# Performance work log

Measured on AMD Instinct MI355X. Metric: run time of the kernel, lower is better.

The kernel has to match this reference:

```python
import jax, jax.numpy as jnp
import numpy as np
from jax import lax

DIM = 192; HEADS = 6; WS = 7; SS = 3; D = H = W = 28
N = WS ** 3            # 343 tokens per window
L = D * H * W          # 21952 tokens
B = 2; HID = 4 * DIM   # 768
SCALE = (DIM // HEADS) ** -0.5
EPS = 1e-5


def _win_part_np(x, ws):
    Bn, Hh, Ww, Tt, C = x.shape
    x = x.reshape(Bn, Hh // ws, ws, Ww // ws, ws, Tt // ws, ws, C)
    return x.transpose(0, 1, 3, 5, 2, 4, 6, 7).reshape(-1, ws, ws, ws, C)


def build_mask():
    # standard Swin shifted-window mask: region ids -> pairwise -100/0
    img = np.zeros((1, D, H, W, 1), np.float32)
    cnt = 0
    sls = (slice(0, -WS), slice(-WS, -SS), slice(-SS, None))
    for a in sls:
        for b in sls:
            for c in sls:
                img[:, a, b, c, :] = cnt
                cnt += 1
    mw = _win_part_np(img, WS).reshape(-1, N)  # (nW, N)
    am = mw[:, None, :] - mw[:, :, None]
    return np.where(am != 0, -100.0, 0.0).astype(np.float32)


def _rel_pos_index():
    coords = np.stack(np.meshgrid(np.arange(WS), np.arange(WS), np.arange(WS), indexing='ij'))
    cf = coords.reshape(3, -1)
    rc = (cf[:, :, None] - cf[:, None, :]).transpose(1, 2, 0)
    rc += WS - 1
    rc[..., 0] *= (2 * WS - 1) ** 2
    rc[..., 1] *= (2 * WS - 1)
    return rc.sum(-1)  # (N, N)

RPI = jnp.asarray(_rel_pos_index())


def setup_inputs() -> dict:
    key = jax.random.key(0)
    ks = jax.random.split(key, 12)
    p = lambda i, shape: jax.random.normal(ks[i], shape, jnp.float32) * 0.02
    return dict(
        x=jax.random.normal(ks[0], (B, L, DIM), jnp.float32),
        mask_matrixx=jnp.asarray(build_mask()),
        norm1_g=jnp.ones((DIM,), jnp.float32), norm1_b=jnp.zeros((DIM,), jnp.float32),
        qkv_w=p(1, (DIM, 3 * DIM)), qkv_b=jnp.zeros((3 * DIM,), jnp.float32),
        rpb=p(2, ((2 * WS - 1) ** 3, HEADS)),
        proj_w=p(3, (DIM, DIM)), proj_b=jnp.zeros((DIM,), jnp.float32),
        norm2_g=jnp.ones((DIM,), jnp.float32), norm2_b=jnp.zeros((DIM,), jnp.float32),
        lin1_w=p(4, (DIM, HID)), lin1_b=jnp.zeros((HID,), jnp.float32),
        lin2_w=p(5, (HID, DIM)), lin2_b=jnp.zeros((DIM,), jnp.float32),
        dw1_k=p(6, (DIM, 1, 3, 3, 3)), dw1_b=jnp.zeros((DIM,), jnp.float32),
        pw1_k=p(7, (DIM, DIM, 1, 1, 1)), pw1_b=jnp.zeros((DIM,), jnp.float32),
        dw2_k=p(8, (DIM, 1, 3, 3, 3)), dw2_b=jnp.zeros((DIM,), jnp.float32),
        pw2_k=p(9, (DIM, DIM, 1, 1, 1)), pw2_b=jnp.zeros((DIM,), jnp.float32),
    )


def _ln(x, g, b):
    m = x.mean(-1, keepdims=True)
    v = ((x - m) ** 2).mean(-1, keepdims=True)
    return (x - m) * lax.rsqrt(v + EPS) * g + b


def _conv3d(x, k, b, groups):
    y = lax.conv_general_dilated(x, k, (1, 1, 1), 'SAME', feature_group_count=groups,
                                 dimension_numbers=('NCDHW', 'OIDHW', 'NCDHW'))
    return y + b.reshape(1, -1, 1, 1, 1)


def reference(x, mask_matrixx, norm1_g, norm1_b, qkv_w, qkv_b, rpb, proj_w, proj_b,
              norm2_g, norm2_b, lin1_w, lin1_b, lin2_w, lin2_b,
              dw1_k, dw1_b, pw1_k, pw1_b, dw2_k, dw2_b, pw2_k, pw2_b):
    shortcut = x
    xn = _ln(x, norm1_g, norm1_b).reshape(B, D, H, W, DIM)
    # cyclic shift (shift_size > 0)
    sx = jnp.roll(xn, (-SS, -SS, -SS), axis=(1, 2, 3))
    # window partition -> (B*nW, N, C)
    xw = sx.reshape(B, D // WS, WS, H // WS, WS, W // WS, WS, DIM)
    xw = xw.transpose(0, 1, 3, 5, 2, 4, 6, 7).reshape(-1, N, DIM)
    Bw = xw.shape[0]
    nW = Bw // B
    hd = DIM // HEADS
    qkv = (xw @ qkv_w + qkv_b).reshape(Bw, N, 3, HEADS, hd).transpose(2, 0, 3, 1, 4)
    q, k, v = qkv[0] * SCALE, qkv[1], qkv[2]
    attn = jnp.einsum('bhnd,bhmd->bhnm', q, k)
    attn = attn + rpb[RPI].transpose(2, 0, 1)[None]          # (1, heads, N, N)
    attn = attn.reshape(B, nW, HEADS, N, N) + mask_matrixx[None, :, None]
    attn = jax.nn.softmax(attn.reshape(Bw, HEADS, N, N), axis=-1)
    out = jnp.einsum('bhnm,bhmd->bhnd', attn, v).transpose(0, 2, 1, 3).reshape(Bw, N, DIM)
    out = out @ proj_w + proj_b
    # window reverse + reverse shift
    out = out.reshape(B, D // WS, H // WS, W // WS, WS, WS, WS, DIM)
    out = out.transpose(0, 1, 4, 2, 5, 3, 6, 7).reshape(B, D, H, W, DIM)
    out = jnp.roll(out, (SS, SS, SS), axis=(1, 2, 3)).reshape(B, L, DIM)
    x = shortcut + out
    # LeFeedForward: linear MLP branch + double depthwise-separable conv3d branch
    xm = _ln(x, norm2_g, norm2_b)
    lin = jax.nn.gelu(xm @ lin1_w + lin1_b, approximate=False) @ lin2_w + lin2_b
    rx = xm.reshape(B, D, H, W, DIM).transpose(0, 4, 1, 2, 3)  # NCDHW
    rx = _conv3d(_conv3d(rx, dw1_k, dw1_b, DIM), pw1_k, pw1_b, 1)
    rx = _conv3d(_conv3d(rx, dw2_k, dw2_b, DIM), pw2_k, pw2_b, 1)
    # original does rx.view(B, -1, dim) on NCDHW-contiguous memory (layout-mixing);
    # jnp.reshape on the same layout replicates it exactly
    rx = rx.reshape(B, -1, DIM)
    return x + (rx + lin)
```

## Files before the change

### kernel.cpp

```cpp
#include <hip/hip_runtime.h>

typedef unsigned short u16;
typedef unsigned int   u32;

#define DIMC 192
#define NWIN 343
#define LTOK 21952
#define ROWSZ 43904
#define TOTE 8429568
#define QSCALE 0.17677669529663689f
#define EPSF 1e-5f

typedef __attribute__((ext_vector_type(8))) short bf16x8v;
typedef __attribute__((ext_vector_type(4))) float f32x4v;

__device__ __forceinline__ float bu(u16 v){ union{u32 u; float f;} x; x.u = ((u32)v)<<16; return x.f; }
__device__ __forceinline__ float lo16(u32 p){ union{u32 u; float f;} x; x.u = p<<16; return x.f; }
__device__ __forceinline__ float hi16(u32 p){ union{u32 u; float f;} x; x.u = p & 0xffff0000u; return x.f; }
__device__ __forceinline__ u16 fb(float f){
  union{float ff; u32 u;} x; x.ff = f;
  u32 r = (x.u + 0x7fffu + ((x.u>>16)&1u)) >> 16;
  return (u16)r;
}
__device__ __forceinline__ float gelu_f(float x){ return 0.5f*x*(1.0f + erff(x*0.70710678118654752f)); }

__device__ __forceinline__ f32x4v mfma_bf16(bf16x8v a, bf16x8v b, f32x4v c){
  return __builtin_amdgcn_mfma_f32_16x16x32_bf16(a, b, c, 0, 0, 0);
}

__device__ __forceinline__ void row_to_token(int row, int& b, int& l){
  int bw = row / NWIN, n = row % NWIN;
  b = bw >> 6; int wi = bw & 63;
  int sd = (wi>>4)*7      + n/49;
  int sh = ((wi>>2)&3)*7  + (n/7)%7;
  int sw = (wi&3)*7       + n%7;
  int d = sd+3; if(d>=28) d-=28;
  int h = sh+3; if(h>=28) h-=28;
  int w = sw+3; if(w>=28) w-=28;
  l = d*784 + h*28 + w;
}

template<int TR>
__global__ __launch_bounds__(256) void pack_w(const float* __restrict__ W, u16* __restrict__ dst,
                                              int K, int N){
  int gid = blockIdx.x*256 + threadIdx.x;
  if(gid >= K*N) return;
  int k = gid / N, n = gid - k*N;
  float v = TR ? W[(long)n*K + k] : W[(long)k*N + n];
  int nt = n >> 4, ks = k >> 5;
  int l  = (((k>>3)&3)<<4) | (n&15);
  int j  = k & 7;
  int KS = K >> 5;
  dst[((((nt*KS + ks)<<6) + l)<<3) + j] = fb(v);
}

__global__ __launch_bounds__(256) void pack_dwk(const float* __restrict__ k1, const float* __restrict__ k2,
                                                float* __restrict__ d1, float* __restrict__ d2){
  int gid = blockIdx.x*256 + threadIdx.x;
  if(gid < 5184){
    int tap = gid/192, c = gid - tap*192;
    d1[gid] = k1[c*27 + tap];
    d2[gid] = k2[c*27 + tap];
  }
}

__global__ __launch_bounds__(256) void ln_win(const float* __restrict__ x, const float* __restrict__ g,
                                              const float* __restrict__ bb, u16* __restrict__ out){
  int row  = blockIdx.x*4 + (threadIdx.x>>6);
  int lane = threadIdx.x & 63;
  int b, l; row_to_token(row, b, l);
  const float* p = x + ((long)b*LTOK + l)*DIMC;
  float v0 = p[lane], v1 = p[lane+64], v2 = p[lane+128];
  float s = v0+v1+v2;
  #pragma unroll
  for(int m=1;m<64;m<<=1) s += __shfl_xor(s,m);
  float mean = s*(1.f/192.f);
  float d0=v0-mean, d1=v1-mean, d2=v2-mean;
  float q = d0*d0+d1*d1+d2*d2;
  #pragma unroll
  for(int m=1;m<64;m<<=1) q += __shfl_xor(q,m);
  float rstd = rsqrtf(q*(1.f/192.f)+EPSF);
  u16* o = out + (long)row*DIMC;
  o[lane]     = fb(d0*rstd*g[lane]     + bb[lane]);
  o[lane+64]  = fb(d1*rstd*g[lane+64]  + bb[lane+64]);
  o[lane+128] = fb(d2*rstd*g[lane+128] + bb[lane+128]);
}

__global__ __launch_bounds__(256) void ln_plain(const u16* __restrict__ in, const float* __restrict__ g,
                                                const float* __restrict__ bb, u16* __restrict__ out){
  int row  = blockIdx.x*4 + (threadIdx.x>>6);
  int lane = threadIdx.x & 63;
  const u16* p = in + (long)row*DIMC;
  float v0 = bu(p[lane]), v1 = bu(p[lane+64]), v2 = bu(p[lane+128]);
  float s = v0+v1+v2;
  #pragma unroll
  for(int m=1;m<64;m<<=1) s += __shfl_xor(s,m);
  float mean = s*(1.f/192.f);
  float d0=v0-mean, d1=v1-mean, d2=v2-mean;
  float q = d0*d0+d1*d1+d2*d2;
  #pragma unroll
  for(int m=1;m<64;m<<=1) q += __shfl_xor(q,m);
  float rstd = rsqrtf(q*(1.f/192.f)+EPSF);
  u16* o = out + (long)row*DIMC;
  o[lane]     = fb(d0*rstd*g[lane]     + bb[lane]);
  o[lane+64]  = fb(d1*rstd*g[lane+64]  + bb[lane+64]);
  o[lane+128] = fb(d2*rstd*g[lane+128] + bb[lane+128]);
}

template<int NTOT, int EPI>
__global__ __launch_bounds__(256) void gemm_mfma(const u16* __restrict__ A, const u16* __restrict__ Wp,
                                                 const float* __restrict__ bias, u16* __restrict__ out,
                                                 const float* __restrict__ resid){
  constexpr int KS  = 6;
  constexpr int NPW = NTOT/64;
  __shared__ u16 As[32*192];
  const int tid = threadIdx.x;
  const int w = tid>>6, l = tid&63;
  const int lm = l&15, lh = l>>4;
  const long row0 = (long)blockIdx.x*32;

  {
    const uint4* src = (const uint4*)(A + row0*192);
    #pragma unroll
    for(int c=0;c<3;c++){
      int cz = tid + c*256;
      int row = cz/24;
      int byte = (cz*16) ^ ((row&7)<<4);
      *(uint4*)((char*)As + byte) = src[cz];
    }
  }
  __syncthreads();

  f32x4v acc[NPW][2];
  const f32x4v z4 = {0.f,0.f,0.f,0.f};
  #pragma unroll
  for(int i=0;i<NPW;i++){ acc[i][0]=z4; acc[i][1]=z4; }

  #pragma unroll
  for(int ks=0;ks<KS;ks++){
    bf16x8v a[2];
    #pragma unroll
    for(int mt=0;mt<2;mt++){
      int row = mt*16 + lm;
      int byte = (row*384 + ks*64 + lh*16) ^ ((row&7)<<4);
      a[mt] = *(const bf16x8v*)((const char*)As + byte);
    }
    #pragma unroll
    for(int i=0;i<NPW;i++){
      int nt = w*NPW + i;
      bf16x8v b = *(const bf16x8v*)(Wp + ((((nt*KS + ks)<<6) + l)<<3));
      acc[i][0] = mfma_bf16(a[0], b, acc[i][0]);
      acc[i][1] = mfma_bf16(a[1], b, acc[i][1]);
    }
  }

  #pragma unroll
  for(int i=0;i<NPW;i++){
    int n = (w*NPW + i)*16 + lm;
    float bv = bias[n];
    #pragma unroll
    for(int mt=0;mt<2;mt++){
      #pragma unroll
      for(int r=0;r<4;r++){
        long mrow = row0 + mt*16 + lh*4 + r;
        float v = acc[i][mt][r] + bv;
        if constexpr(EPI==0){
          out[mrow*NTOT + n] = fb(v);
        } else {
          int b_, lt; row_to_token((int)mrow, b_, lt);
          long li = ((long)b_*LTOK + lt)*DIMC + n;
          out[li] = fb(v + resid[li]);
        }
      }
    }
  }
}

__global__ __launch_bounds__(256) void mlp_mfma(const u16* __restrict__ xm, const u16* __restrict__ Wp1,
                                                const float* __restrict__ b1, const u16* __restrict__ Wp2,
                                                const float* __restrict__ b2, u16* __restrict__ out){
  __shared__ u16 As[32*192];
  __shared__ u16 Hs[32*768];
  const int tid = threadIdx.x;
  const int w = tid>>6, l = tid&63;
  const int lm = l&15, lh = l>>4;
  const long row0 = (long)blockIdx.x*32;

  {
    const uint4* src = (const uint4*)(xm + row0*192);
    #pragma unroll
    for(int c=0;c<3;c++){
      int cz = tid + c*256;
      int row = cz/24;
      int byte = (cz*16) ^ ((row&7)<<4);
      *(uint4*)((char*)As + byte) = src[cz];
    }
  }
  __syncthreads();

  const f32x4v z4 = {0.f,0.f,0.f,0.f};
  f32x4v acc1[12][2];
  #pragma unroll
  for(int i=0;i<12;i++){ acc1[i][0]=z4; acc1[i][1]=z4; }

  #pragma unroll
  for(int ks=0;ks<6;ks++){
    bf16x8v a[2];
    #pragma unroll
    for(int mt=0;mt<2;mt++){
      int row = mt*16 + lm;
      int byte = (row*384 + ks*64 + lh*16) ^ ((row&7)<<4);
      a[mt] = *(const bf16x8v*)((const char*)As + byte);
    }
    #pragma unroll
    for(int i=0;i<12;i++){
      int nt = w*12 + i;
      bf16x8v b = *(const bf16x8v*)(Wp1 + ((((nt*6 + ks)<<6) + l)<<3));
      acc1[i][0] = mfma_bf16(a[0], b, acc1[i][0]);
      acc1[i][1] = mfma_bf16(a[1], b, acc1[i][1]);
    }
  }

  #pragma unroll
  for(int i=0;i<12;i++){
    int n = (w*12 + i)*16 + lm;
    float bv = b1[n];
    #pragma unroll
    for(int mt=0;mt<2;mt++){
      #pragma unroll
      for(int r=0;r<4;r++){
        int mrow = mt*16 + lh*4 + r;
        float h = gelu_f(acc1[i][mt][r] + bv);
        int byte = (mrow*1536 + n*2) ^ ((mrow&7)<<4);
        *(u16*)((char*)Hs + byte) = fb(h);
      }
    }
  }
  __syncthreads();

  f32x4v acc2[3][2];
  #pragma unroll
  for(int i=0;i<3;i++){ acc2[i][0]=z4; acc2[i][1]=z4; }

  #pragma unroll 4
  for(int ks=0;ks<24;ks++){
    bf16x8v a[2];
    #pragma unroll
    for(int mt=0;mt<2;mt++){
      int row = mt*16 + lm;
      int byte = (row*1536 + ks*64 + lh*16) ^ ((row&7)<<4);
      a[mt] = *(const bf16x8v*)((const char*)Hs + byte);
    }
    #pragma unroll
    for(int i=0;i<3;i++){
      int nt = w*3 + i;
      bf16x8v b = *(const bf16x8v*)(Wp2 + ((((nt*24 + ks)<<6) + l)<<3));
      acc2[i][0] = mfma_bf16(a[0], b, acc2[i][0]);
      acc2[i][1] = mfma_bf16(a[1], b, acc2[i][1]);
    }
  }

  #pragma unroll
  for(int i=0;i<3;i++){
    int n = (w*3 + i)*16 + lm;
    float bv = b2[n];
    #pragma unroll
    for(int mt=0;mt<2;mt++){
      #pragma unroll
      for(int r=0;r<4;r++){
        long mrow = row0 + mt*16 + lh*4 + r;
        out[mrow*192 + n] = fb(acc2[i][mt][r] + bv);
      }
    }
  }
}

__global__ __launch_bounds__(256) void attn_mfma(const u16* __restrict__ qkv, const float* __restrict__ rpb,
                                                 u16* __restrict__ out){
  __shared__ u16 Qs[352*32];
  __shared__ u16 Ks2[352*32];
  __shared__ u16 Vt[32*360];
  __shared__ u16 Ps[4][16*360];
  __shared__ float rpb_l[2197];
  __shared__ u16 reg_l[352];

  const int tid = threadIdx.x;
  const int bw = blockIdx.x / 6, hh = blockIdx.x % 6;
  const int wi = bw & 63;
  const long rowbase = (long)bw*NWIN;

  for(int i=tid;i<2197;i+=256) rpb_l[i] = rpb[i*6+hh];
  for(int i2=tid;i2<352;i2+=256){
    int rg = 0;
    if(i2 < 343){
      int sd = (wi>>4)*7      + i2/49;
      int sh = ((wi>>2)&3)*7  + (i2/7)%7;
      int sw = (wi&3)*7       + i2%7;
      int rd = sd<21?0:(sd<25?1:2);
      int rh = sh<21?0:(sh<25?1:2);
      int rw = sw<21?0:(sw<25?1:2);
      rg = rd*9+rh*3+rw;
    }
    reg_l[i2] = (u16)rg;
  }
  if(tid < 144){ ((u32*)Qs)[343*16 + tid] = 0; ((u32*)Ks2)[343*16 + tid] = 0; }
  for(int p2=tid;p2<288;p2+=256){
    int d = p2/9, j = 343 + p2%9; Vt[d*360 + j] = 0;
  }

  for(int p = tid; p < 343*16; p += 256){
    int j = p >> 4, dp = p & 15;
    const u32* src = (const u32*)(qkv + (rowbase + j)*576 + hh*32) + dp;
    ((u32*)Qs)[j*16 + dp]  = src[0];
    ((u32*)Ks2)[j*16 + dp] = src[96];
    u32 vv = src[192];
    Vt[(dp*2)*360 + j]   = (u16)(vv & 0xffffu);
    Vt[(dp*2+1)*360 + j] = (u16)(vv >> 16);
  }
  __syncthreads();

  const int w = tid>>6, l = tid&63;
  const int lm = l&15, lh = l>>4;
  u16* Pw = Ps[w];
  const f32x4v z4 = {0.f,0.f,0.f,0.f};

  for(int it = w; it < 22; it += 4){
    const int i0 = it*16;
    bf16x8v aq = *(const bf16x8v*)(Qs + (i0+lm)*32 + lh*8);
    f32x4v acc[22];
    #pragma unroll
    for(int jt=0;jt<22;jt++){
      bf16x8v bk = *(const bf16x8v*)(Ks2 + (jt*16+lm)*32 + lh*8);
      acc[jt] = mfma_bf16(aq, bk, z4);
    }

    int izr[4], iyr[4], ixr[4], irr[4];
    #pragma unroll
    for(int r=0;r<4;r++){
      int i = i0 + lh*4 + r; if(i>342) i=342;
      izr[r]=i/49; int rem=i-izr[r]*49; iyr[r]=rem/7; ixr[r]=rem-iyr[r]*7;
      irr[r]=reg_l[i];
    }
    #pragma unroll
    for(int jt=0;jt<22;jt++){
      int j = jt*16 + lm;
      int jc = j>342?342:j;
      int jz=jc/49; int rem=jc-jz*49; int jy=rem/7; int jx=rem-jy*7;
      int rj = reg_l[jc];
      bool jok = j<343;
      #pragma unroll
      for(int r=0;r<4;r++){
        float bias = rpb_l[(izr[r]-jz+6)*169 + (iyr[r]-jy+6)*13 + (ixr[r]-jx+6)];
        float v = acc[jt][r]*QSCALE + bias + ((irr[r]==rj)?0.f:-100.f);
        acc[jt][r] = jok ? v : -1e30f;
      }
    }

    float rinv[4];
    #pragma unroll
    for(int r=0;r<4;r++){
      float mx = acc[0][r];
      #pragma unroll
      for(int jt=1;jt<22;jt++) mx = fmaxf(mx, acc[jt][r]);
      #pragma unroll
      for(int m=1;m<16;m<<=1) mx = fmaxf(mx, __shfl_xor(mx, m));
      float sm = 0.f;
      #pragma unroll
      for(int jt=0;jt<22;jt++){ float e = __expf(acc[jt][r]-mx); acc[jt][r]=e; sm += e; }
      #pragma unroll
      for(int m=1;m<16;m<<=1) sm += __shfl_xor(sm, m);
      rinv[r] = 1.0f/sm;
    }

    #pragma unroll
    for(int jt=0;jt<22;jt++){
      int j = jt*16+lm;
      #pragma unroll
      for(int r=0;r<4;r++) Pw[(lh*4+r)*360 + j] = fb(acc[jt][r]);
    }

    f32x4v o0=z4, o1=z4;
    #pragma unroll
    for(int ks=0;ks<11;ks++){
      bf16x8v ap = *(const bf16x8v*)(Pw + lm*360 + ks*32 + lh*8);
      bf16x8v b0 = *(const bf16x8v*)(Vt + lm*360 + ks*32 + lh*8);
      bf16x8v b1 = *(const bf16x8v*)(Vt + (16+lm)*360 + ks*32 + lh*8);
      o0 = mfma_bf16(ap, b0, o0);
      o1 = mfma_bf16(ap, b1, o1);
    }

    #pragma unroll
    for(int r=0;r<4;r++){
      int i = i0 + lh*4 + r;
      if(i < 343){
        u16* po = out + (rowbase + i)*192 + hh*32;
        po[lm]    = fb(o0[r]*rinv[r]);
        po[16+lm] = fb(o1[r]*rinv[r]);
      }
    }
  }
}

__global__ __launch_bounds__(256) void dw3v(const u16* __restrict__ in, const float* __restrict__ kwT,
                                            const float* __restrict__ bias, u16* __restrict__ out){
  __shared__ float wls[5184];
  const int tid = threadIdx.x;
  for(int i=tid;i<5184;i+=256) wls[i] = kwT[i];
  __syncthreads();

  int gid = blockIdx.x*256 + tid;
  int t  = gid / 24, c8 = gid - t*24;
  int b  = t / LTOK, s = t - b*LTOK;
  int z  = s / 784; int r2 = s - z*784; int y = r2/28; int x = r2 - y*28;
  const u16* base = in + (long)t*192 + c8*8;

  float acc[8];
  {
    const float4* bp = (const float4*)(bias + c8*8);
    float4 b0 = bp[0], b1 = bp[1];
    acc[0]=b0.x; acc[1]=b0.y; acc[2]=b0.z; acc[3]=b0.w;
    acc[4]=b1.x; acc[5]=b1.y; acc[6]=b1.z; acc[7]=b1.w;
  }

  #pragma unroll
  for(int dz=-1;dz<=1;dz++){
    int zz=z+dz; if((unsigned)zz>=28u) continue;
    #pragma unroll
    for(int dy=-1;dy<=1;dy++){
      int yy=y+dy; if((unsigned)yy>=28u) continue;
      #pragma unroll
      for(int dx=-1;dx<=1;dx++){
        int xx=x+dx; if((unsigned)xx>=28u) continue;
        int tap = (dz+1)*9+(dy+1)*3+(dx+1);
        uint4 v = *(const uint4*)(base + (long)(dz*784+dy*28+dx)*192);
        const float* wp = &wls[tap*192 + c8*8];
        float4 w0 = *(const float4*)wp;
        float4 w1 = *(const float4*)(wp+4);
        acc[0] = fmaf(lo16(v.x), w0.x, acc[0]);
        acc[1] = fmaf(hi16(v.x), w0.y, acc[1]);
        acc[2] = fmaf(lo16(v.y), w0.z, acc[2]);
        acc[3] = fmaf(hi16(v.y), w0.w, acc[3]);
        acc[4] = fmaf(lo16(v.z), w1.x, acc[4]);
        acc[5] = fmaf(hi16(v.z), w1.y, acc[5]);
        acc[6] = fmaf(lo16(v.w), w1.z, acc[6]);
        acc[7] = fmaf(hi16(v.w), w1.w, acc[7]);
      }
    }
  }

  uint4 o;
  o.x = ((u32)fb(acc[1])<<16) | fb(acc[0]);
  o.y = ((u32)fb(acc[3])<<16) | fb(acc[2]);
  o.z = ((u32)fb(acc[5])<<16) | fb(acc[4]);
  o.w = ((u32)fb(acc[7])<<16) | fb(acc[6]);
  *(uint4*)(out + (long)t*192 + c8*8) = o;
}

__global__ __launch_bounds__(256) void final_add(const u16* __restrict__ x1, const u16* __restrict__ lin,
                                                 const u16* __restrict__ t2, float* __restrict__ out){
  int gid = blockIdx.x*256 + threadIdx.x;
  int b  = gid / 4214784;
  int gg = gid - b*4214784;
  int ch = gg / LTOK;
  int sp = gg - ch*LTOK;
  out[gid] = bu(x1[gid]) + bu(lin[gid]) + bu(t2[((long)b*LTOK + sp)*192 + ch]);
}

extern "C" void kernel_launch(void* const* d_in, const int* in_sizes, int n_in,
                              void* d_out, int out_size, void* d_ws, size_t ws_size,
                              hipStream_t stream){
  const float* x      = (const float*)d_in[0];
  const float* n1g    = (const float*)d_in[2];
  const float* n1b    = (const float*)d_in[3];
  const float* qkv_w  = (const float*)d_in[4];
  const float* qkv_b  = (const float*)d_in[5];
  const float* rpb    = (const float*)d_in[6];
  const float* proj_w = (const float*)d_in[7];
  const float* proj_b = (const float*)d_in[8];
  const float* n2g    = (const float*)d_in[9];
  const float* n2b    = (const float*)d_in[10];
  const float* l1w    = (const float*)d_in[11];
  const float* l1b    = (const float*)d_in[12];
  const float* l2w    = (const float*)d_in[13];
  const float* l2b    = (const float*)d_in[14];
  const float* dw1k   = (const float*)d_in[15];
  const float* dw1b   = (const float*)d_in[16];
  const float* pw1k   = (const float*)d_in[17];
  const float* pw1b   = (const float*)d_in[18];
  const float* dw2k   = (const float*)d_in[19];
  const float* dw2b   = (const float*)d_in[20];
  const float* pw2k   = (const float*)d_in[21];
  const float* pw2b   = (const float*)d_in[22];

  const size_t FB = (size_t)ROWSZ * DIMC;
  u16* x1b   = (u16*)d_ws;
  u16* winb  = x1b + FB;
  u16* attnb = winb + FB;
  u16* qkvb  = attnb + FB;
  u16* cb1   = qkvb;
  u16* cb2   = qkvb + FB;
  u16* xmb   = winb;
  u16* linb  = attnb;
  u16* pk_qkv  = x1b + 6*FB;
  u16* pk_proj = pk_qkv  + 110592;
  u16* pk_l1   = pk_proj + 36864;
  u16* pk_l2   = pk_l1   + 147456;
  u16* pk_pw1  = pk_l2   + 147456;
  u16* pk_pw2  = pk_pw1  + 36864;
  float* kwT1  = (float*)(pk_pw2 + 36864);
  float* kwT2  = kwT1 + 5184;

  pack_w<0><<<432,256,0,stream>>>(qkv_w,  pk_qkv,  192, 576);
  pack_w<0><<<144,256,0,stream>>>(proj_w, pk_proj, 192, 192);
  pack_w<0><<<576,256,0,stream>>>(l1w,    pk_l1,   192, 768);
  pack_w<0><<<576,256,0,stream>>>(l2w,    pk_l2,   768, 192);
  pack_w<1><<<144,256,0,stream>>>(pw1k,   pk_pw1,  192, 192);
  pack_w<1><<<144,256,0,stream>>>(pw2k,   pk_pw2,  192, 192);
  pack_dwk<<<21,256,0,stream>>>(dw1k, dw2k, kwT1, kwT2);

  ln_win<<<ROWSZ/4,256,0,stream>>>(x, n1g, n1b, winb);
  gemm_mfma<576,0><<<ROWSZ/32,256,0,stream>>>(winb, pk_qkv, qkv_b, qkvb, nullptr);
  attn_mfma<<<128*6,256,0,stream>>>(qkvb, rpb, attnb);
  gemm_mfma<192,1><<<ROWSZ/32,256,0,stream>>>(attnb, pk_proj, proj_b, x1b, x);
  ln_plain<<<ROWSZ/4,256,0,stream>>>(x1b, n2g, n2b, xmb);
  mlp_mfma<<<ROWSZ/32,256,0,stream>>>(xmb, pk_l1, l1b, pk_l2, l2b, linb);
  dw3v<<<4116,256,0,stream>>>(xmb, kwT1, dw1b, cb1);
  gemm_mfma<192,0><<<ROWSZ/32,256,0,stream>>>(cb1, pk_pw1, pw1b, cb2, nullptr);
  dw3v<<<4116,256,0,stream>>>(cb2, kwT2, dw2b, cb1);
  gemm_mfma<192,0><<<ROWSZ/32,256,0,stream>>>(cb1, pk_pw2, pw2b, cb2, nullptr);
  final_add<<<TOTE/256,256,0,stream>>>(x1b, linb, cb2, (float*)d_out);
}
```

Measured before the change: 453.1 us.

## Shrink attention LDS footprint: fold Q scale, bf16 bias table, split P buffer

The Q scale factor moves into the QKV GEMM epilogue. The attention kernel then drops its Q shared-memory buffer and reads Q fragments straight from global memory. K is stored pre-swizzled into MFMA fragment order, and the relative-position bias table is held as bf16. Per-token linear indices and region ids are packed so the bias lookup needs a single subtraction instead of div/mod work. The probability buffer is halved by running the PV product in two chunks. Together these cut LDS use enough to fit more blocks per CU. The costs are bf16 rounding of the bias, and the last tile of the last window reading Q rows slightly past the end of the buffer.

```diff
diff --git a/kernel.cpp b/kernel.cpp
--- a/kernel.cpp
+++ b/kernel.cpp
@@ -107,7 +107,7 @@
   o[lane+128] = fb(d2*rstd*g[lane+128] + bb[lane+128]);
 }
 
-template<int NTOT, int EPI>
+template<int NTOT, int EPI, int QS = 0>
 __global__ __launch_bounds__(256) void gemm_mfma(const u16* __restrict__ A, const u16* __restrict__ Wp,
                                                  const float* __restrict__ bias, u16* __restrict__ out,
                                                  const float* __restrict__ resid){
@@ -164,6 +164,7 @@
       for(int r=0;r<4;r++){
         long mrow = row0 + mt*16 + lh*4 + r;
         float v = acc[i][mt][r] + bv;
+        if constexpr(QS){ if(n < 192) v *= QSCALE; }
         if constexpr(EPI==0){
           out[mrow*NTOT + n] = fb(v);
         } else {
@@ -277,33 +278,30 @@
 
 __global__ __launch_bounds__(256) void attn_mfma(const u16* __restrict__ qkv, const float* __restrict__ rpb,
                                                  u16* __restrict__ out){
-  __shared__ u16 Qs[352*32];
-  __shared__ u16 Ks2[352*32];
+  __shared__ u16 Kf[22*512];
   __shared__ u16 Vt[32*360];
-  __shared__ u16 Ps[4][16*360];
-  __shared__ float rpb_l[2197];
-  __shared__ u16 reg_l[352];
+  __shared__ u16 Ps[4][16*200];
+  __shared__ u16 rpb_l[2198];
+  __shared__ u32 lin_l[352];
 
   const int tid = threadIdx.x;
   const int bw = blockIdx.x / 6, hh = blockIdx.x % 6;
   const int wi = bw & 63;
   const long rowbase = (long)bw*NWIN;
 
-  for(int i=tid;i<2197;i+=256) rpb_l[i] = rpb[i*6+hh];
+  for(int i=tid;i<2197;i+=256) rpb_l[i] = fb(rpb[i*6+hh]);
   for(int i2=tid;i2<352;i2+=256){
-    int rg = 0;
+    u32 v = 0x7FFF0000u;
     if(i2 < 343){
-      int sd = (wi>>4)*7      + i2/49;
-      int sh = ((wi>>2)&3)*7  + (i2/7)%7;
-      int sw = (wi&3)*7       + i2%7;
+      int jz = i2/49, jr = i2-jz*49, jy = jr/7, jx = jr-jy*7;
+      int sd = (wi>>4)*7 + jz, sh2 = ((wi>>2)&3)*7 + jy, sw = (wi&3)*7 + jx;
       int rd = sd<21?0:(sd<25?1:2);
-      int rh = sh<21?0:(sh<25?1:2);
+      int rh = sh2<21?0:(sh2<25?1:2);
       int rw = sw<21?0:(sw<25?1:2);
-      rg = rd*9+rh*3+rw;
-    }
-    reg_l[i2] = (u16)rg;
-  }
-  if(tid < 144){ ((u32*)Qs)[343*16 + tid] = 0; ((u32*)Ks2)[343*16 + tid] = 0; }
+      v = (u32)(jz*169 + jy*13 + jx) | ((u32)(rd*9+rh*3+rw)<<16);
+    }
+    lin_l[i2] = v;
+  }
   for(int p2=tid;p2<288;p2+=256){
     int d = p2/9, j = 343 + p2%9; Vt[d*360 + j] = 0;
   }
@@ -311,9 +309,9 @@
   for(int p = tid; p < 343*16; p += 256){
     int j = p >> 4, dp = p & 15;
     const u32* src = (const u32*)(qkv + (rowbase + j)*576 + hh*32) + dp;
-    ((u32*)Qs)[j*16 + dp]  = src[0];
-    ((u32*)Ks2)[j*16 + dp] = src[96];
+    u32 kk = src[96];
     u32 vv = src[192];
+    ((u32*)Kf)[(j>>4)*256 + ((dp>>2)*16 + (j&15))*4 + (dp&3)] = kk;
     Vt[(dp*2)*360 + j]   = (u16)(vv & 0xffffu);
     Vt[(dp*2+1)*360 + j] = (u16)(vv >> 16);
   }
@@ -326,32 +324,30 @@
 
   for(int it = w; it < 22; it += 4){
     const int i0 = it*16;
-    bf16x8v aq = *(const bf16x8v*)(Qs + (i0+lm)*32 + lh*8);
+    bf16x8v aq = *(const bf16x8v*)(qkv + (rowbase + i0 + lm)*576 + hh*32 + lh*8);
+
     f32x4v acc[22];
     #pragma unroll
     for(int jt=0;jt<22;jt++){
-      bf16x8v bk = *(const bf16x8v*)(Ks2 + (jt*16+lm)*32 + lh*8);
+      bf16x8v bk = *(const bf16x8v*)(Kf + jt*512 + l*8);
       acc[jt] = mfma_bf16(aq, bk, z4);
     }
 
-    int izr[4], iyr[4], ixr[4], irr[4];
+    u32 li[4];
     #pragma unroll
     for(int r=0;r<4;r++){
       int i = i0 + lh*4 + r; if(i>342) i=342;
-      izr[r]=i/49; int rem=i-izr[r]*49; iyr[r]=rem/7; ixr[r]=rem-iyr[r]*7;
-      irr[r]=reg_l[i];
+      li[r] = lin_l[i];
     }
     #pragma unroll
     for(int jt=0;jt<22;jt++){
-      int j = jt*16 + lm;
-      int jc = j>342?342:j;
-      int jz=jc/49; int rem=jc-jz*49; int jy=rem/7; int jx=rem-jy*7;
-      int rj = reg_l[jc];
-      bool jok = j<343;
+      u32 lj = lin_l[jt*16 + lm];
+      bool jok = (jt*16 + lm) < 343;
+      int ljl = (int)(lj & 0xffffu); u32 ljr = lj >> 16;
       #pragma unroll
       for(int r=0;r<4;r++){
-        float bias = rpb_l[(izr[r]-jz+6)*169 + (iyr[r]-jy+6)*13 + (ixr[r]-jx+6)];
-        float v = acc[jt][r]*QSCALE + bias + ((irr[r]==rj)?0.f:-100.f);
+        int idx = (int)(li[r] & 0xffffu) - ljl + 1098;
+        float v = acc[jt][r] + bu(rpb_l[idx]) + (((li[r]>>16)==ljr) ? 0.f : -100.f);
         acc[jt][r] = jok ? v : -1e30f;
       }
     }
@@ -372,19 +368,32 @@
       rinv[r] = 1.0f/sm;
     }
 
-    #pragma unroll
-    for(int jt=0;jt<22;jt++){
-      int j = jt*16+lm;
-      #pragma unroll
-      for(int r=0;r<4;r++) Pw[(lh*4+r)*360 + j] = fb(acc[jt][r]);
-    }
-
     f32x4v o0=z4, o1=z4;
     #pragma unroll
-    for(int ks=0;ks<11;ks++){
-      bf16x8v ap = *(const bf16x8v*)(Pw + lm*360 + ks*32 + lh*8);
+    for(int jt=0;jt<12;jt++){
+      int jl = jt*16 + lm;
+      #pragma unroll
+      for(int r=0;r<4;r++) Pw[(lh*4+r)*200 + jl] = fb(acc[jt][r]);
+    }
+    #pragma unroll
+    for(int ks=0;ks<6;ks++){
+      bf16x8v ap = *(const bf16x8v*)(Pw + lm*200 + ks*32 + lh*8);
       bf16x8v b0 = *(const bf16x8v*)(Vt + lm*360 + ks*32 + lh*8);
       bf16x8v b1 = *(const bf16x8v*)(Vt + (16+lm)*360 + ks*32 + lh*8);
+      o0 = mfma_bf16(ap, b0, o0);
+      o1 = mfma_bf16(ap, b1, o1);
+    }
+    #pragma unroll
+    for(int jt=12;jt<22;jt++){
+      int jl = jt*16 + lm - 192;
+      #pragma unroll
+      for(int r=0;r<4;r++) Pw[(lh*4+r)*200 + jl] = fb(acc[jt][r]);
+    }
+    #pragma unroll
+    for(int ks=0;ks<5;ks++){
+      bf16x8v ap = *(const bf16x8v*)(Pw + lm*200 + ks*32 + lh*8);
+      bf16x8v b0 = *(const bf16x8v*)(Vt + lm*360 + 192 + ks*32 + lh*8);
+      bf16x8v b1 = *(const bf16x8v*)(Vt + (16+lm)*360 + 192 + ks*32 + lh*8);
       o0 = mfma_bf16(ap, b0, o0);
       o1 = mfma_bf16(ap, b1, o1);
     }
@@ -519,7 +528,7 @@
   pack_dwk<<<21,256,0,stream>>>(dw1k, dw2k, kwT1, kwT2);
 
   ln_win<<<ROWSZ/4,256,0,stream>>>(x, n1g, n1b, winb);
-  gemm_mfma<576,0><<<ROWSZ/32,256,0,stream>>>(winb, pk_qkv, qkv_b, qkvb, nullptr);
+  gemm_mfma<576,0,1><<<ROWSZ/32,256,0,stream>>>(winb, pk_qkv, qkv_b, qkvb, nullptr);
   attn_mfma<<<128*6,256,0,stream>>>(qkvb, rpb, attnb);
   gemm_mfma<192,1><<<ROWSZ/32,256,0,stream>>>(attnb, pk_proj, proj_b, x1b, x);
   ln_plain<<<ROWSZ/4,256,0,stream>>>(x1b, n2g, n2b, xmb);
```

Result: faster. 421.0 us (-7.1%).
